# Kernel tuning notes

Measured on AMD Instinct MI355X. Metric: run time of the kernel, lower is better.

## Reference

```python
import jax, jax.numpy as jnp
import numpy as np

N, E, D, L, G = 50000, 800000, 96, 4, 256
FI, PI, EI = 128, 16, 16


def setup_inputs() -> dict:
    key = jax.random.key(0)
    ks = jax.random.split(key, 40)
    w = lambda k, s: (jax.random.normal(k, s, jnp.float32) * 0.02)
    inp = {
        'h': jax.random.normal(ks[0], (N, FI), jnp.float32),
        'e': jax.random.normal(ks[1], (E, EI), jnp.float32),
        'p': jax.random.normal(ks[2], (N, PI), jnp.float32),
        'edge_index': jax.random.randint(ks[3], (2, E), 0, N),
        'batch': jnp.sort(jax.random.randint(ks[4], (N,), 0, G)),
        # embedding linears
        'h_emb_w': w(ks[5], (FI, D)), 'h_emb_b': jnp.zeros((D,), jnp.float32),
        'e_emb_w': w(ks[6], (EI, D)), 'e_emb_b': jnp.zeros((D,), jnp.float32),
        'p_emb_w': w(ks[7], (PI, D)), 'p_emb_b': jnp.zeros((D,), jnp.float32),
        # per-layer weights, stacked over L layers
        'gate_w': w(ks[8], (L, 3 * D, D)), 'gate_b': jnp.zeros((L, D), jnp.float32),
        'hps_w': w(ks[9], (L, 2 * D, D)), 'hps_b': jnp.zeros((L, D), jnp.float32),
        'hpr_w': w(ks[10], (L, 2 * D, D)), 'hpr_b': jnp.zeros((L, D), jnp.float32),
        'ps_w': w(ks[11], (L, D, D)), 'ps_b': jnp.zeros((L, D), jnp.float32),
        'pr_w': w(ks[12], (L, D, D)), 'pr_b': jnp.zeros((L, D), jnp.float32),
        # readout MLP
        'ro1_w': w(ks[13], (2 * D, D)), 'ro1_b': jnp.zeros((D,), jnp.float32),
        'ro2_w': w(ks[14], (D, 1)), 'ro2_b': jnp.zeros((1,), jnp.float32),
    }
    return inp


def reference(h, e, p, edge_index, batch,
              h_emb_w, h_emb_b, e_emb_w, e_emb_b, p_emb_w, p_emb_b,
              gate_w, gate_b, hps_w, hps_b, hpr_w, hpr_b,
              ps_w, ps_b, pr_w, pr_b, ro1_w, ro1_b, ro2_w, ro2_b):
    send, rec = edge_index[0], edge_index[1]
    n_nodes = h.shape[0]
    h = h @ h_emb_w + h_emb_b
    e = e @ e_emb_w + e_emb_b
    p = p @ p_emb_w + p_emb_b
    n_layers = gate_w.shape[0]
    for l in range(n_layers):
        # gather h at send/rec, gate over concat [E, 3D]
        eta_hat = jax.nn.sigmoid(
            jnp.concatenate([h[send], h[rec], e], axis=1) @ gate_w[l] + gate_b[l])
        eta = eta_hat / jnp.sum(eta_hat, axis=1, keepdims=True)
        hp = jnp.concatenate([h, p], axis=1)  # [N, 2D]
        h_msg = eta * (hp[send] @ hps_w[l] + hps_b[l])
        h_agg = jax.ops.segment_sum(h_msg, rec, num_segments=n_nodes)
        h_new = hp @ hpr_w[l] + hpr_b[l] + h_agg
        p_msg = eta * (p[send] @ ps_w[l] + ps_b[l])
        p_agg = jax.ops.segment_sum(p_msg, rec, num_segments=n_nodes)
        p_new = h_new @ pr_w[l] + pr_b[l] + p_agg  # uses updated h (matches torch layer)
        h = h + jax.nn.relu(h_new)
        e = e + jax.nn.relu(eta_hat)
        p = p + jnp.tanh(p_new)
    h_pool = jax.ops.segment_sum(h, batch, num_segments=G)  # global_add_pool
    p_pool = jax.ops.segment_sum(p, batch, num_segments=G)
    x = jnp.concatenate([h_pool, p_pool], axis=1) @ ro1_w + ro1_b
    x = jax.nn.relu(x) @ ro2_w + ro2_b
    return x.squeeze(-1)  # [G]
```

## Files before the change

### kernel.cpp

```cpp
#include <hip/hip_runtime.h>

typedef unsigned short u16;
typedef unsigned int u32;

#define NN 50000
#define EE 800000
#define DD 96
#define LL 4
#define GG 256
#define NPW 8
#define NPB (4*NPW)

typedef __bf16 bf16x8 __attribute__((ext_vector_type(8)));
typedef float f32x4 __attribute__((ext_vector_type(4)));

__device__ __forceinline__ u16 f2bf(float x){
  u32 u = __float_as_uint(x);
  u32 r = (u + 0x7FFFu + ((u >> 16) & 1u)) >> 16;
  return (u16)r;
}
__device__ __forceinline__ float bf2f(u16 b){
  return __uint_as_float(((u32)b) << 16);
}
union BQ { uint4 q; bf16x8 v; };
__device__ __forceinline__ bf16x8 asbf(uint4 q){ BQ u; u.q = q; return u.v; }
__device__ __forceinline__ f32x4 mfma16(uint4 a, uint4 b, f32x4 c){
  return __builtin_amdgcn_mfma_f32_16x16x32_bf16(asbf(a), asbf(b), c, 0, 0, 0);
}
__device__ __forceinline__ uint4 pack8(const float* v){
  uint4 q;
  q.x = (u32)f2bf(v[0]) | ((u32)f2bf(v[1]) << 16);
  q.y = (u32)f2bf(v[2]) | ((u32)f2bf(v[3]) << 16);
  q.z = (u32)f2bf(v[4]) | ((u32)f2bf(v[5]) << 16);
  q.w = (u32)f2bf(v[6]) | ((u32)f2bf(v[7]) << 16);
  return q;
}
__device__ __forceinline__ uint4 packrow(const float* hsrc, const float* psrc, int row, int kbase){
  const float* src = (kbase < 96) ? (hsrc + (size_t)row*96 + kbase)
                                  : (psrc + (size_t)row*96 + (kbase - 96));
  float4 a0 = ((const float4*)src)[0];
  float4 a1 = ((const float4*)src)[1];
  float v[8] = {a0.x,a0.y,a0.z,a0.w,a1.x,a1.y,a1.z,a1.w};
  return pack8(v);
}

__global__ void k_diag(float* out, float val){
  int i = blockIdx.x*64 + threadIdx.x;
  if (i < GG) out[i] = val;
}

__global__ void k_zero(int* counts){
  int i = blockIdx.x*256 + threadIdx.x;
  if (i < NN) counts[i] = 0;
}
__global__ void k_hist(const int* rec, int* counts){
  int e = blockIdx.x*256 + threadIdx.x;
  if (e < EE) atomicAdd(&counts[rec[e]], 1);
}
__global__ void k_scan(const int* counts, int* cursor, int* node_start){
  __shared__ int wsum[16];
  __shared__ int carry_s;
  const int tid = threadIdx.x, lane = tid & 63, wid = tid >> 6;
  if (tid == 0) carry_s = 0;
  __syncthreads();
  for (int base = 0; base < NN; base += 1024){
    int i = base + tid;
    int v = (i < NN) ? counts[i] : 0;
    int x = v;
    #pragma unroll
    for (int d = 1; d < 64; d <<= 1){
      int t = __shfl_up(x, d);
      if (lane >= d) x += t;
    }
    if (lane == 63) wsum[wid] = x;
    __syncthreads();
    if (wid == 0 && lane < 16){
      int y = wsum[lane];
      #pragma unroll
      for (int d = 1; d < 16; d <<= 1){ int t = __shfl_up(y, d); if (lane >= d) y += t; }
      wsum[lane] = y;
    }
    __syncthreads();
    int woff = (wid == 0) ? 0 : wsum[wid-1];
    if (i < NN){
      int ex = carry_s + woff + x - v;
      cursor[i] = ex;
      node_start[i] = ex;
    }
    __syncthreads();
    if (tid == 1023) carry_s += wsum[15];
    __syncthreads();
  }
  if (tid == 0) node_start[NN] = EE;
}
__global__ void k_scatter(const int* send, const int* rec, int* cursor,
                          int* ss, int* rs, int* perm){
  int e = blockIdx.x*256 + threadIdx.x;
  if (e >= EE) return;
  int r = rec[e];
  int pos = atomicAdd(&cursor[r], 1);
  ss[pos] = send[e];
  rs[pos] = r;
  perm[pos] = e;
}

__global__ void k_prep(const float* gate_w, const float* gate_b,
    const float* hps_w, const float* hps_b,
    const float* hpr_w, const float* hpr_b,
    const float* ps_w, const float* ps_b,
    const float* pr_w,
    const float* h_emb_w, const float* p_emb_w, const float* e_emb_w,
    u16* Wt_cat, float* bias_cat, u16* Wt_e, u16* Wt_pr, u16* Wt_emb, u16* Wt_ee){
  int i = blockIdx.x*256 + threadIdx.x;
  const int S0 = LL*480*192, S1 = LL*96*96, S2 = LL*96*96, S3 = 192*160, S4 = 96*32, S5 = LL*480;
  if (i < S0){
    int l = i / (480*192); int r = i % (480*192);
    int j = r / 192, k = r % 192;
    int g = j / 96, jj = j % 96;
    float v = 0.f;
    if (g == 0){ if (k < 96) v = gate_w[((size_t)l*288 + k)*96 + jj]; }
    else if (g == 1){ if (k < 96) v = gate_w[((size_t)l*288 + 96 + k)*96 + jj]; }
    else if (g == 2){ if (k >= 96) v = ps_w[((size_t)l*96 + (k-96))*96 + jj]; }
    else if (g == 3){ v = hps_w[((size_t)l*192 + k)*96 + jj]; }
    else            { v = hpr_w[((size_t)l*192 + k)*96 + jj]; }
    Wt_cat[i] = f2bf(v);
    return;
  }
  i -= S0;
  if (i < S1){
    int l = i / 9216, r = i % 9216; int j = r / 96, k = r % 96;
    Wt_e[i] = f2bf(gate_w[((size_t)l*288 + 192 + k)*96 + j]);
    return;
  }
  i -= S1;
  if (i < S2){
    int l = i / 9216, r = i % 9216; int j = r / 96, k = r % 96;
    Wt_pr[i] = f2bf(pr_w[((size_t)l*96 + k)*96 + j]);
    return;
  }
  i -= S2;
  if (i < S3){
    int j = i / 160, k = i % 160;
    float v = 0.f;
    if (j < 96){ if (k < 128) v = h_emb_w[k*96 + j]; }
    else { if (k >= 128 && k < 144) v = p_emb_w[(k-128)*96 + (j-96)]; }
    Wt_emb[i] = f2bf(v);
    return;
  }
  i -= S3;
  if (i < S4){
    int j = i / 32, k = i % 32;
    Wt_ee[i] = f2bf(k < 16 ? e_emb_w[k*96 + j] : 0.f);
    return;
  }
  i -= S4;
  if (i < S5){
    int l = i / 480, j = i % 480;
    int g = j / 96, jj = j % 96;
    float v = 0.f;
    if (g == 1) v = gate_b[l*96 + jj];
    else if (g == 2) v = ps_b[l*96 + jj];
    else if (g == 3) v = hps_b[l*96 + jj];
    else if (g == 4) v = hpr_b[l*96 + jj];
    bias_cat[i] = v;
  }
}

__global__ __launch_bounds__(256,2) void k_emb_hp(const float* h_in, const float* p_in,
    const u16* Wt_emb, const float* h_emb_b, const float* p_emb_b,
    float* h, float* p){
  __shared__ u16 lds[96*168];
  const int tid = threadIdx.x;
  const int j0 = blockIdx.y * 96;
  for (int c = tid; c < 96*160/8; c += 256){
    int jr = c / 20, kc = c % 20;
    *(uint4*)&lds[jr*168 + kc*8] = *(const uint4*)(Wt_emb + (size_t)(j0+jr)*160 + kc*8);
  }
  __syncthreads();
  const int wave = tid >> 6, lane = tid & 63;
  const int quad = lane >> 4, l15 = lane & 15;
  const int base = blockIdx.x*256 + wave*64;
  f32x4 zero = {0.f,0.f,0.f,0.f};
  f32x4 acc[4][6];
  #pragma unroll
  for (int rg=0; rg<4; ++rg){
    #pragma unroll
    for (int ct=0; ct<6; ++ct) acc[rg][ct] = zero;
  }
  for (int ks = 0; ks < 5; ++ks){
    uint4 aq[4];
    #pragma unroll
    for (int rg = 0; rg < 4; ++rg){
      int row = base + rg*16 + l15;
      int chunk = ks*4 + quad;
      float v[8] = {0.f,0.f,0.f,0.f,0.f,0.f,0.f,0.f};
      if (row < NN){
        if (chunk < 16){
          const float4* sp = (const float4*)(h_in + (size_t)row*128 + chunk*8);
          float4 a0 = sp[0], a1 = sp[1];
          v[0]=a0.x; v[1]=a0.y; v[2]=a0.z; v[3]=a0.w; v[4]=a1.x; v[5]=a1.y; v[6]=a1.z; v[7]=a1.w;
        } else if (chunk < 18){
          const float4* sp = (const float4*)(p_in + (size_t)row*16 + (chunk-16)*8);
          float4 a0 = sp[0], a1 = sp[1];
          v[0]=a0.x; v[1]=a0.y; v[2]=a0.z; v[3]=a0.w; v[4]=a1.x; v[5]=a1.y; v[6]=a1.z; v[7]=a1.w;
        }
      }
      aq[rg] = pack8(v);
    }
    #pragma unroll
    for (int ct = 0; ct < 6; ++ct){
      uint4 bq = *(const uint4*)&lds[(ct*16+l15)*168 + ks*32 + quad*8];
      #pragma unroll
      for (int rg = 0; rg < 4; ++rg) acc[rg][ct] = mfma16(aq[rg], bq, acc[rg][ct]);
    }
  }
  #pragma unroll
  for (int rg=0; rg<4; ++rg){
    #pragma unroll
    for (int ct=0; ct<6; ++ct){
      #pragma unroll
      for (int reg=0; reg<4; ++reg){
        int row = base + rg*16 + quad*4 + reg;
        if (row < NN){
          int col = j0 + ct*16 + l15;
          float v = acc[rg][ct][reg] + (col < 96 ? h_emb_b[col] : p_emb_b[col-96]);
          if (col < 96) h[(size_t)row*96 + col] = v;
          else          p[(size_t)row*96 + col - 96] = v;
        }
      }
    }
  }
}

__global__ __launch_bounds__(256,2) void k_emb_e(const float* e_in, const int* perm,
    const u16* Wt_ee, const float* e_emb_b, u16* e_bf){
  __shared__ u16 lds[96*40];
  const int tid = threadIdx.x;
  for (int c = tid; c < 96*32/8; c += 256){
    int jr = c >> 2, kc = c & 3;
    *(uint4*)&lds[jr*40 + kc*8] = *(const uint4*)(Wt_ee + jr*32 + kc*8);
  }
  __syncthreads();
  const int wave = tid >> 6, lane = tid & 63;
  const int quad = lane >> 4, l15 = lane & 15;
  const int base = blockIdx.x*256 + wave*64;
  f32x4 zero = {0.f,0.f,0.f,0.f};
  f32x4 acc[4][6];
  #pragma unroll
  for (int rg=0; rg<4; ++rg){
    #pragma unroll
    for (int ct=0; ct<6; ++ct) acc[rg][ct] = zero;
  }
  uint4 aq[4];
  #pragma unroll
  for (int rg = 0; rg < 4; ++rg){
    int row = base + rg*16 + l15;
    int src = perm[row];
    float v[8] = {0.f,0.f,0.f,0.f,0.f,0.f,0.f,0.f};
    if (quad < 2){
      const float4* sp = (const float4*)(e_in + (size_t)src*16 + quad*8);
      float4 a0 = sp[0], a1 = sp[1];
      v[0]=a0.x; v[1]=a0.y; v[2]=a0.z; v[3]=a0.w; v[4]=a1.x; v[5]=a1.y; v[6]=a1.z; v[7]=a1.w;
    }
    aq[rg] = pack8(v);
  }
  #pragma unroll
  for (int ct = 0; ct < 6; ++ct){
    uint4 bq = *(const uint4*)&lds[(ct*16+l15)*40 + quad*8];
    #pragma unroll
    for (int rg = 0; rg < 4; ++rg) acc[rg][ct] = mfma16(aq[rg], bq, acc[rg][ct]);
  }
  #pragma unroll
  for (int rg=0; rg<4; ++rg){
    #pragma unroll
    for (int ct=0; ct<6; ++ct){
      #pragma unroll
      for (int reg=0; reg<4; ++reg){
        int row = base + rg*16 + quad*4 + reg;
        int col = ct*16 + l15;
        e_bf[(size_t)row*96 + col] = f2bf(acc[rg][ct][reg] + e_emb_b[col]);
      }
    }
  }
}

__global__ __launch_bounds__(256,2) void k_pre(const float* h, const float* p,
    const u16* Wt_cat, const float* bias_cat, int l,
    u16* G, float* h_agg){
  __shared__ u16 lds[96*200];
  const int tid = threadIdx.x;
  const int group = blockIdx.y;
  const u16* W = Wt_cat + ((size_t)l*480 + group*96)*192;
  for (int c = tid; c < 96*192/8; c += 256){
    int jr = c / 24, kc = c % 24;
    *(uint4*)&lds[jr*200 + kc*8] = *(const uint4*)(W + jr*192 + kc*8);
  }
  __syncthreads();
  const int wave = tid >> 6, lane = tid & 63;
  const int quad = lane >> 4, l15 = lane & 15;
  const int base = blockIdx.x*256 + wave*64;
  f32x4 zero = {0.f,0.f,0.f,0.f};
  f32x4 acc[4][6];
  #pragma unroll
  for (int rg=0; rg<4; ++rg){
    #pragma unroll
    for (int ct=0; ct<6; ++ct) acc[rg][ct] = zero;
  }
  const int ks0 = (group == 2) ? 3 : 0;
  const int ks1 = (group <= 1) ? 3 : 6;
  uint4 zeroq = {0u,0u,0u,0u};
  for (int ks = ks0; ks < ks1; ++ks){
    int kbase = ks*32 + quad*8;
    uint4 aq[4];
    #pragma unroll
    for (int rg = 0; rg < 4; ++rg){
      int row = base + rg*16 + l15;
      aq[rg] = (row < NN) ? packrow(h, p, row, kbase) : zeroq;
    }
    #pragma unroll
    for (int ct = 0; ct < 6; ++ct){
      uint4 bq = *(const uint4*)&lds[(ct*16+l15)*200 + ks*32 + quad*8];
      #pragma unroll
      for (int rg = 0; rg < 4; ++rg) acc[rg][ct] = mfma16(aq[rg], bq, acc[rg][ct]);
    }
  }
  const float* bptr = bias_cat + l*480 + group*96;
  #pragma unroll
  for (int rg=0; rg<4; ++rg){
    #pragma unroll
    for (int ct=0; ct<6; ++ct){
      #pragma unroll
      for (int reg=0; reg<4; ++reg){
        int row = base + rg*16 + quad*4 + reg;
        if (row < NN){
          int col = ct*16 + l15;
          float v = acc[rg][ct][reg] + bptr[col];
          if (group == 4) h_agg[(size_t)row*96 + col] = v;
          else            G[(size_t)row*384 + group*96 + col] = f2bf(v);
        }
      }
    }
  }
}

__global__ __launch_bounds__(256,3) void k_edge(u16* e_bf, const u16* Wt_e_l,
    const int* ss, const int* rs, const int* node_start,
    const u16* G, float* h_agg, float* p_agg){
  __shared__ u16 lds[96*104];
  __shared__ float accLDS[4][2][NPW*96];
  const int tid = threadIdx.x;
  for (int c = tid; c < 96*96/8; c += 256){
    int jr = c / 12, kc = c % 12;
    *(uint4*)&lds[jr*104 + kc*8] = *(const uint4*)(Wt_e_l + jr*96 + kc*8);
  }
  __syncthreads();
  const int wave = tid >> 6, lane = tid & 63;
  const int quad = lane >> 4, l15 = lane & 15;
  const int n0 = blockIdx.x*NPB + wave*NPW;
  if (n0 >= NN) return;
  const int n1 = min(n0 + NPW, NN);
  const int ws0 = node_start[n0], ws1 = node_start[n1];
  float* accH = accLDS[wave][0];
  float* accP = accLDS[wave][1];
  for (int k = lane; k < NPW*96; k += 64){ accH[k] = 0.f; accP[k] = 0.f; }

  for (int tb = ws0; tb < ws1; tb += 64){
    f32x4 zero = {0.f,0.f,0.f,0.f};
    f32x4 acc[4][6];
    #pragma unroll
    for (int rg=0; rg<4; ++rg){
      #pragma unroll
      for (int ct=0; ct<6; ++ct) acc[rg][ct] = zero;
    }
    #pragma unroll
    for (int ks = 0; ks < 3; ++ks){
      uint4 aq[4];
      #pragma unroll
      for (int rg = 0; rg < 4; ++rg){
        int row = tb + rg*16 + l15;
        if (row > EE-1) row = EE-1;
        aq[rg] = *(const uint4*)(e_bf + (size_t)row*96 + ks*32 + quad*8);
      }
      #pragma unroll
      for (int ct = 0; ct < 6; ++ct){
        uint4 bq = *(const uint4*)&lds[(ct*16+l15)*104 + ks*32 + quad*8];
        #pragma unroll
        for (int rg = 0; rg < 4; ++rg) acc[rg][ct] = mfma16(aq[rg], bq, acc[rg][ct]);
      }
    }
    #pragma unroll
    for (int rg=0; rg<4; ++rg){
      const int e0 = tb + rg*16 + quad*4;
      if (e0 >= ws1) continue;
      float hacc[6], pacc[6], Grv[6];
      #pragma unroll
      for (int ct=0; ct<6; ++ct){ hacc[ct]=0.f; pacc[ct]=0.f; }
      int curR = rs[e0];
      {
        const u16* Gr = G + (size_t)curR*384 + 96;
        #pragma unroll
        for (int ct=0; ct<6; ++ct) Grv[ct] = bf2f(Gr[ct*16 + l15]);
      }
      #pragma unroll
      for (int reg=0; reg<4; ++reg){
        const int edge = e0 + reg;
        if (edge < ws1){
          const int s = ss[edge], r = rs[edge];
          if (r != curR){
            int nb = (curR - n0)*96;
            #pragma unroll
            for (int ct=0; ct<6; ++ct){
              int col = ct*16 + l15;
              atomicAdd(&accH[nb+col], hacc[ct]);
              atomicAdd(&accP[nb+col], pacc[ct]);
              hacc[ct]=0.f; pacc[ct]=0.f;
            }
            curR = r;
            const u16* Gr = G + (size_t)curR*384 + 96;
            #pragma unroll
            for (int ct=0; ct<6; ++ct) Grv[ct] = bf2f(Gr[ct*16 + l15]);
          }
          const u16* Gs = G + (size_t)s*384;
          float eh[6]; float rsum = 0.f;
          #pragma unroll
          for (int ct=0; ct<6; ++ct){
            int col = ct*16 + l15;
            float z = acc[rg][ct][reg] + bf2f(Gs[col]) + Grv[ct];
            float v = 1.f/(1.f + __expf(-z));
            eh[ct] = v; rsum += v;
          }
          rsum += __shfl_xor(rsum, 1); rsum += __shfl_xor(rsum, 2);
          rsum += __shfl_xor(rsum, 4); rsum += __shfl_xor(rsum, 8);
          float inv = 1.f / rsum;
          #pragma unroll
          for (int ct=0; ct<6; ++ct){
            int col = ct*16 + l15;
            size_t ei = (size_t)edge*96 + col;
            e_bf[ei] = f2bf(bf2f(e_bf[ei]) + eh[ct]);
            float eta = eh[ct] * inv;
            hacc[ct] += eta * bf2f(Gs[288 + col]);
            pacc[ct] += eta * bf2f(Gs[192 + col]);
          }
        }
      }
      {
        int nb = (curR - n0)*96;
        #pragma unroll
        for (int ct=0; ct<6; ++ct){
          int col = ct*16 + l15;
          atomicAdd(&accH[nb+col], hacc[ct]);
          atomicAdd(&accP[nb+col], pacc[ct]);
        }
      }
    }
  }
  const int nk = (n1 - n0)*96;
  for (int k = lane; k < nk; k += 64){
    size_t gi = (size_t)n0*96 + k;
    h_agg[gi] += accH[k];
    p_agg[gi]  = accP[k];
  }
}

__global__ void k_nodeA(const float* h_agg, float* h){
  int i = blockIdx.x*256 + threadIdx.x;
  if (i >= NN*96) return;
  h[i] += fmaxf(h_agg[i], 0.f);
}

__global__ __launch_bounds__(256,2) void k_pr(const float* h_agg, const u16* Wt_pr_l,
    const float* pr_b_l, const float* p_agg, float* p){
  __shared__ u16 lds[96*104];
  const int tid = threadIdx.x;
  for (int c = tid; c < 96*96/8; c += 256){
    int jr = c / 12, kc = c % 12;
    *(uint4*)&lds[jr*104 + kc*8] = *(const uint4*)(Wt_pr_l + jr*96 + kc*8);
  }
  __syncthreads();
  const int wave = tid >> 6, lane = tid & 63;
  const int quad = lane >> 4, l15 = lane & 15;
  const int base = blockIdx.x*256 + wave*64;
  f32x4 zero = {0.f,0.f,0.f,0.f};
  f32x4 acc[4][6];
  #pragma unroll
  for (int rg=0; rg<4; ++rg){
    #pragma unroll
    for (int ct=0; ct<6; ++ct) acc[rg][ct] = zero;
  }
  uint4 zeroq = {0u,0u,0u,0u};
  #pragma unroll
  for (int ks = 0; ks < 3; ++ks){
    int kbase = ks*32 + quad*8;
    uint4 aq[4];
    #pragma unroll
    for (int rg = 0; rg < 4; ++rg){
      int row = base + rg*16 + l15;
      aq[rg] = (row < NN) ? packrow(h_agg, h_agg, row, kbase) : zeroq;
    }
    #pragma unroll
    for (int ct = 0; ct < 6; ++ct){
      uint4 bq = *(const uint4*)&lds[(ct*16+l15)*104 + ks*32 + quad*8];
      #pragma unroll
      for (int rg = 0; rg < 4; ++rg) acc[rg][ct] = mfma16(aq[rg], bq, acc[rg][ct]);
    }
  }
  #pragma unroll
  for (int rg=0; rg<4; ++rg){
    #pragma unroll
    for (int ct=0; ct<6; ++ct){
      #pragma unroll
      for (int reg=0; reg<4; ++reg){
        int row = base + rg*16 + quad*4 + reg;
        if (row < NN){
          int col = ct*16 + l15;
          float v = acc[rg][ct][reg] + pr_b_l[col] + p_agg[(size_t)row*96+col];
          float vv = fminf(fmaxf(v, -15.f), 15.f);
          float ex = __expf(2.f*vv);
          float th = (ex - 1.f) / (ex + 1.f);
          p[(size_t)row*96+col] += th;
        }
      }
    }
  }
}

__global__ void k_off(const int* batch, int* starts){
  int g = threadIdx.x;
  int lo = 0, hi = NN;
  while (lo < hi){ int mid = (lo + hi) >> 1; if (batch[mid] < g) lo = mid + 1; else hi = mid; }
  starts[g] = lo;
  if (g == 0) starts[GG] = NN;
}

__global__ void k_pool(const float* h, const float* p, const int* starts, float* pool){
  int g = blockIdx.x, t = threadIdx.x;
  int a = starts[g], b = starts[g+1];
  const float* src = (t < 96) ? h : p;
  int c = (t < 96) ? t : (t - 96);
  float s = 0.f;
  for (int n = a; n < b; ++n) s += src[(size_t)n*96 + c];
  pool[g*192 + t] = s;
}

__global__ void k_ro(const float* pool, const float* ro1_w, const float* ro1_b,
                     const float* ro2_w, const float* ro2_b, float* out){
  __shared__ float red[96];
  int g = blockIdx.x, j = threadIdx.x;
  if (j < 96){
    float a = ro1_b[j];
    for (int k = 0; k < 192; ++k) a += pool[g*192 + k] * ro1_w[k*96 + j];
    red[j] = fmaxf(a, 0.f) * ro2_w[j];
  }
  __syncthreads();
  if (j == 0){
    float s = 0.f;
    for (int k = 0; k < 96; ++k) s += red[k];
    out[g] = s + ro2_b[0];
  }
}

extern "C" void kernel_launch(void* const* d_in, const int* in_sizes, int n_in,
                              void* d_out, int out_size, void* d_ws, size_t ws_size,
                              hipStream_t stream){
  const float* in_h    = (const float*)d_in[0];
  const float* in_e    = (const float*)d_in[1];
  const float* in_p    = (const float*)d_in[2];
  const int*   eidx    = (const int*)d_in[3];
  const int*   batch   = (const int*)d_in[4];
  const float* h_emb_w = (const float*)d_in[5];
  const float* h_emb_b = (const float*)d_in[6];
  const float* e_emb_w = (const float*)d_in[7];
  const float* e_emb_b = (const float*)d_in[8];
  const float* p_emb_w = (const float*)d_in[9];
  const float* p_emb_b = (const float*)d_in[10];
  const float* gate_w  = (const float*)d_in[11];
  const float* gate_b  = (const float*)d_in[12];
  const float* hps_w   = (const float*)d_in[13];
  const float* hps_b   = (const float*)d_in[14];
  const float* hpr_w   = (const float*)d_in[15];
  const float* hpr_b   = (const float*)d_in[16];
  const float* ps_w    = (const float*)d_in[17];
  const float* ps_b    = (const float*)d_in[18];
  const float* pr_w    = (const float*)d_in[19];
  const float* pr_b    = (const float*)d_in[20];
  const float* ro1_w   = (const float*)d_in[21];
  const float* ro1_b   = (const float*)d_in[22];
  const float* ro2_w   = (const float*)d_in[23];
  const float* ro2_b   = (const float*)d_in[24];
  float* out = (float*)d_out;
  (void)in_sizes; (void)n_in; (void)out_size;

  u16* G = (u16*)d_in[1];

  char* w = (char*)d_ws;
  size_t off = 0;
  auto alloc = [&](size_t bytes)->char*{
    char* pt = w + off;
    off = (off + bytes + 255) & ~(size_t)255;
    return pt;
  };
  u16*   e_bf     = (u16*)alloc((size_t)EE*96*2);
  float* h        = (float*)alloc((size_t)NN*96*4);
  float* p        = (float*)alloc((size_t)NN*96*4);
  float* h_agg    = (float*)alloc((size_t)NN*96*4);
  float* p_agg    = (float*)alloc((size_t)NN*96*4);
  u16*   Wt_cat   = (u16*)alloc((size_t)LL*480*192*2);
  u16*   Wt_e     = (u16*)alloc((size_t)LL*96*96*2);
  u16*   Wt_pr    = (u16*)alloc((size_t)LL*96*96*2);
  float* bias_cat = (float*)alloc((size_t)LL*480*4);
  int*   perm     = (int*)alloc((size_t)EE*4);
  int*   ss       = (int*)alloc((size_t)EE*4);
  int*   rs       = (int*)alloc((size_t)EE*4);
  int*   counts   = (int*)alloc((size_t)NN*4);
  int*   cursor   = (int*)alloc((size_t)NN*4);
  int*   node_start = (int*)alloc((size_t)(NN+1)*4);
  char*  scratch  = alloc(197888);
  u16*   Wt_emb   = (u16*)scratch;
  u16*   Wt_ee    = (u16*)(scratch + 61440);
  float* pool     = (float*)scratch;
  int*   starts   = (int*)(scratch + 196608);
  const size_t NEED = off;

  if (ws_size < NEED){
    k_diag<<<4, 64, 0, stream>>>(out, (float)(ws_size >> 20));
    return;
  }

  const int* send = eidx;
  const int* rec  = eidx + EE;

  k_zero<<<196, 256, 0, stream>>>(counts);
  k_hist<<<3125, 256, 0, stream>>>(rec, counts);
  k_scan<<<1, 1024, 0, stream>>>(counts, cursor, node_start);
  k_scatter<<<3125, 256, 0, stream>>>(send, rec, cursor, ss, rs, perm);

  k_prep<<<1868, 256, 0, stream>>>(gate_w, gate_b, hps_w, hps_b, hpr_w, hpr_b,
      ps_w, ps_b, pr_w, h_emb_w, p_emb_w, e_emb_w,
      Wt_cat, bias_cat, Wt_e, Wt_pr, Wt_emb, Wt_ee);
  k_emb_hp<<<dim3(196,2), 256, 0, stream>>>(in_h, in_p, Wt_emb, h_emb_b, p_emb_b, h, p);
  k_emb_e<<<3125, 256, 0, stream>>>(in_e, perm, Wt_ee, e_emb_b, e_bf);

  const int edge_blocks = (NN + NPB - 1) / NPB;
  for (int l = 0; l < LL; ++l){
    k_pre<<<dim3(196,5), 256, 0, stream>>>(h, p, Wt_cat, bias_cat, l, G, h_agg);
    k_edge<<<edge_blocks, 256, 0, stream>>>(e_bf, Wt_e + (size_t)l*96*96, ss, rs,
                                            node_start, G, h_agg, p_agg);
    k_nodeA<<<18750, 256, 0, stream>>>(h_agg, h);
    k_pr<<<196, 256, 0, stream>>>(h_agg, Wt_pr + (size_t)l*96*96, pr_b + l*96, p_agg, p);
  }

  k_off<<<1, 256, 0, stream>>>(batch, starts);
  k_pool<<<GG, 192, 0, stream>>>(h, p, starts, pool);
  k_ro<<<GG, 128, 0, stream>>>(pool, ro1_w, ro1_b, ro2_w, ro2_b, out);
}
```

Before: 2.411 ms.

## Repack gate projections into per-lane vector layout and fuse h update into k_pr

k_pre now writes the per-node projections into a padded [N,512] bf16 layout. Each lane's six columns for a group sit contiguously, so k_edge gathers sender and receiver rows with single 16-byte loads instead of many scalar 2-byte loads. Sender and receiver indices are also read as int4 vectors. The separate elementwise k_nodeA launch is folded into k_pr's epilogue, which saves one pass over h and h_agg and one launch per layer. The costs are a larger padded intermediate, about a third more bytes written, and an assumption that the edge offsets are 16-byte aligned for the int4 index loads.

After: 2.416 ms. About the same (+0.2%).

```diff
diff --git a/kernel.cpp b/kernel.cpp
--- a/kernel.cpp
+++ b/kernel.cpp
@@ -21,6 +21,11 @@
 }
 __device__ __forceinline__ float bf2f(u16 b){
   return __uint_as_float(((u32)b) << 16);
+}
+__device__ __forceinline__ float bfx(const uint4& q, int i){
+  u32 w = (i < 2) ? q.x : (i < 4) ? q.y : (i < 6) ? q.z : q.w;
+  u32 h = (i & 1) ? (w >> 16) : (w & 0xFFFFu);
+  return __uint_as_float(h << 16);
 }
 union BQ { uint4 q; bf16x8 v; };
 __device__ __forceinline__ bf16x8 asbf(uint4 q){ BQ u; u.q = q; return u.v; }
@@ -286,7 +291,7 @@
 
 __global__ __launch_bounds__(256,2) void k_pre(const float* h, const float* p,
     const u16* Wt_cat, const float* bias_cat, int l,
-    u16* G, float* h_agg){
+    u16* Gt, float* h_agg){
   __shared__ u16 lds[96*200];
   const int tid = threadIdx.x;
   const int group = blockIdx.y;
@@ -325,18 +330,36 @@
     }
   }
   const float* bptr = bias_cat + l*480 + group*96;
-  #pragma unroll
-  for (int rg=0; rg<4; ++rg){
-    #pragma unroll
-    for (int ct=0; ct<6; ++ct){
+  if (group == 4){
+    #pragma unroll
+    for (int rg=0; rg<4; ++rg){
+      #pragma unroll
+      for (int ct=0; ct<6; ++ct){
+        #pragma unroll
+        for (int reg=0; reg<4; ++reg){
+          int row = base + rg*16 + quad*4 + reg;
+          if (row < NN){
+            int col = ct*16 + l15;
+            h_agg[(size_t)row*96 + col] = acc[rg][ct][reg] + bptr[col];
+          }
+        }
+      }
+    }
+  } else {
+    float bv[6];
+    #pragma unroll
+    for (int ct=0; ct<6; ++ct) bv[ct] = bptr[ct*16 + l15];
+    #pragma unroll
+    for (int rg=0; rg<4; ++rg){
       #pragma unroll
       for (int reg=0; reg<4; ++reg){
         int row = base + rg*16 + quad*4 + reg;
         if (row < NN){
-          int col = ct*16 + l15;
-          float v = acc[rg][ct][reg] + bptr[col];
-          if (group == 4) h_agg[(size_t)row*96 + col] = v;
-          else            G[(size_t)row*384 + group*96 + col] = f2bf(v);
+          float v[8];
+          #pragma unroll
+          for (int ct=0; ct<6; ++ct) v[ct] = acc[rg][ct][reg] + bv[ct];
+          v[6] = 0.f; v[7] = 0.f;
+          *(uint4*)(Gt + (size_t)row*512 + group*128 + l15*8) = pack8(v);
         }
       }
     }
@@ -345,7 +368,7 @@
 
 __global__ __launch_bounds__(256,3) void k_edge(u16* e_bf, const u16* Wt_e_l,
     const int* ss, const int* rs, const int* node_start,
-    const u16* G, float* h_agg, float* p_agg){
+    const u16* Gt, float* h_agg, float* p_agg){
   __shared__ u16 lds[96*104];
   __shared__ float accLDS[4][2][NPW*96];
   const int tid = threadIdx.x;
@@ -392,20 +415,20 @@
     for (int rg=0; rg<4; ++rg){
       const int e0 = tb + rg*16 + quad*4;
       if (e0 >= ws1) continue;
-      float hacc[6], pacc[6], Grv[6];
+      int4 s4 = *(const int4*)(ss + e0);
+      int4 r4 = *(const int4*)(rs + e0);
+      const int sArr[4] = {s4.x, s4.y, s4.z, s4.w};
+      const int rArr[4] = {r4.x, r4.y, r4.z, r4.w};
+      float hacc[6], pacc[6];
       #pragma unroll
       for (int ct=0; ct<6; ++ct){ hacc[ct]=0.f; pacc[ct]=0.f; }
-      int curR = rs[e0];
-      {
-        const u16* Gr = G + (size_t)curR*384 + 96;
-        #pragma unroll
-        for (int ct=0; ct<6; ++ct) Grv[ct] = bf2f(Gr[ct*16 + l15]);
-      }
+      int curR = rArr[0];
+      uint4 grq = *(const uint4*)(Gt + (size_t)curR*512 + 128 + l15*8);
       #pragma unroll
       for (int reg=0; reg<4; ++reg){
         const int edge = e0 + reg;
         if (edge < ws1){
-          const int s = ss[edge], r = rs[edge];
+          const int s = sArr[reg], r = rArr[reg];
           if (r != curR){
             int nb = (curR - n0)*96;
             #pragma unroll
@@ -416,16 +439,16 @@
               hacc[ct]=0.f; pacc[ct]=0.f;
             }
             curR = r;
-            const u16* Gr = G + (size_t)curR*384 + 96;
-            #pragma unroll
-            for (int ct=0; ct<6; ++ct) Grv[ct] = bf2f(Gr[ct*16 + l15]);
+            grq = *(const uint4*)(Gt + (size_t)curR*512 + 128 + l15*8);
           }
-          const u16* Gs = G + (size_t)s*384;
+          const u16* Gs = Gt + (size_t)s*512 + l15*8;
+          uint4 aqv = *(const uint4*)(Gs);
+          uint4 sqv = *(const uint4*)(Gs + 256);
+          uint4 mqv = *(const uint4*)(Gs + 384);
           float eh[6]; float rsum = 0.f;
           #pragma unroll
           for (int ct=0; ct<6; ++ct){
-            int col = ct*16 + l15;
-            float z = acc[rg][ct][reg] + bf2f(Gs[col]) + Grv[ct];
+            float z = acc[rg][ct][reg] + bfx(aqv, ct) + bfx(grq, ct);
             float v = 1.f/(1.f + __expf(-z));
             eh[ct] = v; rsum += v;
           }
@@ -438,8 +461,8 @@
             size_t ei = (size_t)edge*96 + col;
             e_bf[ei] = f2bf(bf2f(e_bf[ei]) + eh[ct]);
             float eta = eh[ct] * inv;
-            hacc[ct] += eta * bf2f(Gs[288 + col]);
-            pacc[ct] += eta * bf2f(Gs[192 + col]);
+            hacc[ct] += eta * bfx(mqv, ct);
+            pacc[ct] += eta * bfx(sqv, ct);
           }
         }
       }
@@ -462,14 +485,8 @@
   }
 }
 
-__global__ void k_nodeA(const float* h_agg, float* h){
-  int i = blockIdx.x*256 + threadIdx.x;
-  if (i >= NN*96) return;
-  h[i] += fmaxf(h_agg[i], 0.f);
-}
-
 __global__ __launch_bounds__(256,2) void k_pr(const float* h_agg, const u16* Wt_pr_l,
-    const float* pr_b_l, const float* p_agg, float* p){
+    const float* pr_b_l, const float* p_agg, float* p, float* h){
   __shared__ u16 lds[96*104];
   const int tid = threadIdx.x;
   for (int c = tid; c < 96*96/8; c += 256){
@@ -513,11 +530,13 @@
         int row = base + rg*16 + quad*4 + reg;
         if (row < NN){
           int col = ct*16 + l15;
-          float v = acc[rg][ct][reg] + pr_b_l[col] + p_agg[(size_t)row*96+col];
+          size_t idx = (size_t)row*96 + col;
+          float v = acc[rg][ct][reg] + pr_b_l[col] + p_agg[idx];
           float vv = fminf(fmaxf(v, -15.f), 15.f);
           float ex = __expf(2.f*vv);
           float th = (ex - 1.f) / (ex + 1.f);
-          p[(size_t)row*96+col] += th;
+          p[idx] += th;
+          h[idx] += fmaxf(h_agg[idx], 0.f);
         }
       }
     }
@@ -590,7 +609,7 @@
   float* out = (float*)d_out;
   (void)in_sizes; (void)n_in; (void)out_size;
 
-  u16* G = (u16*)d_in[1];
+  u16* Gt = (u16*)d_in[1];
 
   char* w = (char*)d_ws;
   size_t off = 0;
@@ -642,11 +661,11 @@
 
   const int edge_blocks = (NN + NPB - 1) / NPB;
   for (int l = 0; l < LL; ++l){
-    k_pre<<<dim3(196,5), 256, 0, stream>>>(h, p, Wt_cat, bias_cat, l, G, h_agg);
+    k_pre<<<dim3(196,5), 256, 0, stream>>>(h, p, Wt_cat, bias_cat, l, Gt, h_agg);
     k_edge<<<edge_blocks, 256, 0, stream>>>(e_bf, Wt_e + (size_t)l*96*96, ss, rs,
-                                            node_start, G, h_agg, p_agg);
-    k_nodeA<<<18750, 256, 0, stream>>>(h_agg, h);
-    k_pr<<<196, 256, 0, stream>>>(h_agg, Wt_pr + (size_t)l*96*96, pr_b + l*96, p_agg, p);
+                                            node_start, Gt, h_agg, p_agg);
+    k_pr<<<196, 256, 0, stream>>>(h_agg, Wt_pr + (size_t)l*96*96, pr_b + l*96,
+                                  p_agg, p, h);
   }
 
   k_off<<<1, 256, 0, stream>>>(batch, starts);
```
